# Performance work log

Measured on AMD Instinct MI355X. Metric: run time of the kernel, lower is better.

Reference implementation:

```python
import jax, jax.numpy as jnp
import numpy as np

B, N, H = 16, 8192, 128
TOK_MLP, CH_MLP = 256, 512
EPS = 1e-5


def _layer_norm(z, g, b):
    m = jnp.mean(z, axis=-1, keepdims=True)
    v = jnp.mean(jnp.square(z - m), axis=-1, keepdims=True)
    return (z - m) * jax.lax.rsqrt(v + EPS) * g + b


def setup_inputs() -> dict:
    key = jax.random.key(0)
    ks = jax.random.split(key, 9)
    s = 0.02
    return {
        "x": jax.random.normal(ks[0], (B, N, H), dtype=jnp.float32),
        "ln1_g": jnp.ones((H,), jnp.float32),
        "ln1_b": jnp.zeros((H,), jnp.float32),
        "ln2_g": jnp.ones((H,), jnp.float32),
        "ln2_b": jnp.zeros((H,), jnp.float32),
        "tok_w1": jax.random.normal(ks[1], (N, TOK_MLP), jnp.float32) * s,
        "tok_b1": jnp.zeros((TOK_MLP,), jnp.float32),
        "tok_w2": jax.random.normal(ks[2], (TOK_MLP, N), jnp.float32) * s,
        "tok_b2": jnp.zeros((N,), jnp.float32),
        "ch_w1": jax.random.normal(ks[3], (H, CH_MLP), jnp.float32) * s,
        "ch_b1": jnp.zeros((CH_MLP,), jnp.float32),
        "ch_w2": jax.random.normal(ks[4], (CH_MLP, H), jnp.float32) * s,
        "ch_b2": jnp.zeros((H,), jnp.float32),
    }


def reference(x, ln1_g, ln1_b, ln2_g, ln2_b,
              tok_w1, tok_b1, tok_w2, tok_b2,
              ch_w1, ch_b1, ch_w2, ch_b2):
    # x: [B, N, H]
    y = _layer_norm(x, ln1_g, ln1_b)
    # mask-expand-multiply-sum over dim=2 == reverse (suffix) cumsum over tokens:
    # out[b, j, h] = sum_{i >= j} y[b, i, h]
    y = jnp.flip(jnp.cumsum(jnp.flip(y, axis=1), axis=1), axis=1)  # [B, N, H]
    y = jnp.swapaxes(y, 1, 2)                                      # [B, H, N]
    h = jax.nn.gelu(y @ tok_w1 + tok_b1, approximate=False)        # [B, H, TOK_MLP]
    y = h @ tok_w2 + tok_b2                                        # [B, H, N]
    y = jnp.swapaxes(y, 1, 2)                                      # [B, N, H]
    y = _layer_norm(y, ln2_g, ln2_b)
    h = jax.nn.gelu(y @ ch_w1 + ch_b1, approximate=False)          # [B, N, CH_MLP]
    return h @ ch_w2 + ch_b2                                       # [B, N, H]
```

## Files before the change

### kernel.cpp

```cpp
#include <hip/hip_runtime.h>
#include <math.h>

#define B_ 16
#define N_ 8192
#define H_ 128
#define T_ 256
#define C_ 512

typedef __bf16 bf16x8 __attribute__((ext_vector_type(8)));
typedef __bf16 bf16x4 __attribute__((ext_vector_type(4)));
typedef float f32x4 __attribute__((ext_vector_type(4)));

__device__ __forceinline__ float gelu_f(float x) {
    float p = fmaf(0.044715f * x * x, x, x);
    float e = __expf(-1.5957691216057308f * p);
    return x * __builtin_amdgcn_rcpf(1.f + e);
}

__device__ __forceinline__ unsigned short f2bf(float x) {
    unsigned int u = __float_as_uint(x);
    u = (u + 0x7FFFu + ((u >> 16) & 1u)) >> 16;
    return (unsigned short)u;
}

__device__ __forceinline__ void gl2lds16(const void* g, void* l) {
    __builtin_amdgcn_global_load_lds(
        (const __attribute__((address_space(1))) void*)g,
        (__attribute__((address_space(3))) void*)l,
        16, 0, 0);
}

__global__ void k_w1_psum(const float* __restrict__ w1, float* __restrict__ psum) {
    int c = blockIdx.x, t = threadIdx.x;
    const float* p = w1 + (size_t)c * 64 * T_ + t;
    float s = 0.f;
    #pragma unroll 8
    for (int r = 0; r < 64; ++r) s += p[(size_t)r * T_];
    psum[c * T_ + t] = s;
}

__global__ void k_w1_scan(const float* __restrict__ psum, float* __restrict__ offs) {
    int t = threadIdx.x;
    float run = 0.f;
    for (int c = 0; c < 128; ++c) {
        offs[c * T_ + t] = run;
        run += psum[c * T_ + t];
    }
}

__global__ void k_w1_prefix(const float* __restrict__ w1, const float* __restrict__ offs,
                            unsigned short* __restrict__ w1ct) {
    int c = blockIdx.x, t = threadIdx.x;
    float run = offs[c * T_ + t];
    const float* p = w1 + (size_t)c * 64 * T_ + t;
    unsigned int wb[32];
    #pragma unroll
    for (int q = 0; q < 32; ++q) {
        run += p[(size_t)(2 * q) * T_];
        unsigned int lo = f2bf(run);
        run += p[(size_t)(2 * q + 1) * T_];
        wb[q] = lo | ((unsigned int)f2bf(run) << 16);
    }
    char* row = (char*)w1ct + ((size_t)t * N_ + c * 64) * 2;
    int key = (t & 7) << 4;
    #pragma unroll
    for (int pc = 0; pc < 8; ++pc) {
        int4 v = { (int)wb[4*pc], (int)wb[4*pc+1], (int)wb[4*pc+2], (int)wb[4*pc+3] };
        *(int4*)(row + ((pc * 16) ^ key)) = v;
    }
}

__global__ void k_packs(const float* __restrict__ w2, unsigned short* __restrict__ w2t,
                        const float* __restrict__ cw1, const float* __restrict__ cw2,
                        unsigned short* __restrict__ w1p, unsigned short* __restrict__ w2p) {
    __shared__ float ld[64 * 68];
    int tid = threadIdx.x;
    if (blockIdx.y < 4) {
        int nt = blockIdx.x, tt = blockIdx.y;
        int n0 = nt * 64, t0 = tt * 64;
        #pragma unroll
        for (int rnd = 0; rnd < 4; ++rnd) {
            int idx = tid + rnd * 256;
            int tr = idx >> 4, nc = idx & 15;
            float4 v = *(const float4*)(w2 + (size_t)(t0 + tr) * N_ + n0 + nc * 4);
            *(float4*)&ld[tr * 68 + nc * 4] = v;
        }
        __syncthreads();
        int n = tid >> 2, q = tid & 3;
        int key = (n & 7) << 4;
        unsigned int wb[8];
        #pragma unroll
        for (int j = 0; j < 8; ++j) {
            float a = ld[(q * 16 + 2 * j) * 68 + n];
            float b = ld[(q * 16 + 2 * j + 1) * 68 + n];
            wb[j] = (unsigned int)f2bf(a) | ((unsigned int)f2bf(b) << 16);
        }
        char* row = (char*)w2t + (size_t)(n0 + n) * 512 + t0 * 2;
        int4 v0 = { (int)wb[0], (int)wb[1], (int)wb[2], (int)wb[3] };
        int4 v1 = { (int)wb[4], (int)wb[5], (int)wb[6], (int)wb[7] };
        *(int4*)(row + ((q * 32) ^ key)) = v0;
        *(int4*)(row + ((q * 32 + 16) ^ key)) = v1;
    } else {
        int e = ((blockIdx.y - 4) * 128 + blockIdx.x) * 256 + tid;
        if (e < 65536) {
            int c = e >> 13, t = e & 8191;
            int n = t >> 7, j = t & 127;
            int k = j ^ ((n & 7) << 3);
            int hid = c * 64 + n;
            w1p[e] = f2bf(cw1[(size_t)k * C_ + hid]);
        } else {
            int e2 = e - 65536;
            int c = e2 >> 13, t = e2 & 8191;
            int n = t >> 6, j = t & 63;
            int k = j ^ ((n & 7) << 3);
            w2p[e2] = f2bf(cw2[(size_t)(c * 64 + k) * H_ + n]);
        }
    }
}

#define T1_YS 0
#define T1_WS 16384
#define T1_LN 81920

__global__ __launch_bounds__(1024, 1)
void k_tok1(const float* __restrict__ x, const float* __restrict__ lg,
            const float* __restrict__ lb, const unsigned short* __restrict__ w1ct,
            float* __restrict__ P) {
    __shared__ __align__(16) char sm[115712];
    float* lnb = (float*)(sm + T1_LN);
    int kk = blockIdx.x, b = blockIdx.y;
    int tid = threadIdx.x;
    int w = tid >> 6, lane = tid & 63;
    int lr = lane & 15, lk = lane >> 4;
    int mg = w >> 2, ng = w & 3;
    const char* wbg = (const char*)w1ct;
    int kbase = kk * 512;

    int rI = tid >> 4, lI = tid & 15;
    int hII = tid >> 3, segII = tid & 7;
    const float* xbase = x + ((size_t)b * N_ + kbase) * H_;

    float4 g0 = *(const float4*)(lg + lI * 8);
    float4 g1 = *(const float4*)(lg + lI * 8 + 4);
    float4 c0 = *(const float4*)(lb + lI * 8);
    float4 c1 = *(const float4*)(lb + lI * 8 + 4);

    f32x4 acc[2][4];
    #pragma unroll
    for (int i = 0; i < 2; ++i)
        #pragma unroll
        for (int j = 0; j < 4; ++j) acc[i][j] = (f32x4){0.f, 0.f, 0.f, 0.f};

    float4 xa, xb;
    auto XLOAD = [&](int t) {
        const float* p = xbase + (size_t)(t * 64 + rI) * H_ + lI * 8;
        xa = *(const float4*)p;
        xb = *(const float4*)(p + 4);
    };
    auto LNW = [&]() {
        float s1 = xa.x + xa.y + xa.z + xa.w + xb.x + xb.y + xb.z + xb.w;
        float s2 = xa.x*xa.x + xa.y*xa.y + xa.z*xa.z + xa.w*xa.w
                 + xb.x*xb.x + xb.y*xb.y + xb.z*xb.z + xb.w*xb.w;
        #pragma unroll
        for (int off = 1; off < 16; off <<= 1) {
            s1 += __shfl_xor(s1, off);
            s2 += __shfl_xor(s2, off);
        }
        float mean = s1 * (1.f / 128.f);
        float rstd = rsqrtf(s2 * (1.f / 128.f) - mean * mean + 1e-5f);
        float4 o0, o1;
        o0.x = (xa.x - mean) * rstd * g0.x + c0.x;
        o0.y = (xa.y - mean) * rstd * g0.y + c0.y;
        o0.z = (xa.z - mean) * rstd * g0.z + c0.z;
        o0.w = (xa.w - mean) * rstd * g0.w + c0.w;
        o1.x = (xb.x - mean) * rstd * g1.x + c1.x;
        o1.y = (xb.y - mean) * rstd * g1.y + c1.y;
        o1.z = (xb.z - mean) * rstd * g1.z + c1.z;
        o1.w = (xb.w - mean) * rstd * g1.w + c1.w;
        *(float4*)&lnb[rI * 132 + lI * 8]     = o0;
        *(float4*)&lnb[rI * 132 + lI * 8 + 4] = o1;
    };
    auto COLW = [&]() {
        unsigned int d[4];
        #pragma unroll
        for (int j = 0; j < 4; ++j) {
            float a = lnb[(segII * 8 + 2 * j) * 132 + hII];
            float c = lnb[(segII * 8 + 2 * j + 1) * 132 + hII];
            d[j] = (unsigned int)f2bf(a) | ((unsigned int)f2bf(c) << 16);
        }
        int4 v = { (int)d[0], (int)d[1], (int)d[2], (int)d[3] };
        *(int4*)(sm + T1_YS + hII * 128 + ((segII * 16) ^ ((hII & 7) << 4))) = v;
    };
    auto STAGEW = [&](int s, char* buf) {
        int n0 = kbase + s * 64;
        #pragma unroll
        for (int rnd = 0; rnd < 2; ++rnd) {
            int idx = tid + rnd * 1024;
            int tr = idx >> 3, pp = idx & 7;
            gl2lds16(wbg + ((size_t)tr * N_ + n0) * 2 + pp * 16, buf + idx * 16);
        }
    };

    STAGEW(0, sm + T1_WS);
    XLOAD(0);

    for (int s = 0; s < 8; ++s) {
        LNW();
        if (s < 7) XLOAD(s + 1);
        __syncthreads();
        COLW();
        __syncthreads();
        if (s < 7) STAGEW(s + 1, sm + T1_WS + ((s + 1) & 1) * 32768);
        const char* wsb = sm + T1_WS + (s & 1) * 32768;
        #pragma unroll
        for (int ks = 0; ks < 2; ++ks) {
            bf16x8 af[2], bfr[4];
            #pragma unroll
            for (int i = 0; i < 2; ++i) {
                int h = mg * 32 + i * 16 + lr;
                af[i] = *(const bf16x8*)(sm + T1_YS + h * 128 + ((ks * 64 + lk * 16) ^ ((h & 7) << 4)));
            }
            #pragma unroll
            for (int j = 0; j < 4; ++j) {
                int t = ng * 64 + j * 16 + lr;
                bfr[j] = *(const bf16x8*)(wsb + t * 128 + ((ks * 64 + lk * 16) ^ ((t & 7) << 4)));
            }
            #pragma unroll
            for (int i = 0; i < 2; ++i)
                #pragma unroll
                for (int j = 0; j < 4; ++j)
                    acc[i][j] = __builtin_amdgcn_mfma_f32_16x16x32_bf16(af[i], bfr[j], acc[i][j], 0, 0, 0);
        }
        __syncthreads();
    }

    float* Pb = P + ((size_t)(b * 16 + kk)) * (H_ * T_);
    #pragma unroll
    for (int i = 0; i < 2; ++i)
        #pragma unroll
        for (int j = 0; j < 4; ++j) {
            int t = ng * 64 + j * 16 + lr;
            #pragma unroll
            for (int r = 0; r < 4; ++r) {
                int h = mg * 32 + i * 16 + lk * 4 + r;
                Pb[h * T_ + t] = acc[i][j][r];
            }
        }
}

__global__ void k_tok1_fin(const float* __restrict__ P, const float* __restrict__ b1,
                           unsigned short* __restrict__ g1b) {
    int fid = blockIdx.x * 256 + threadIdx.x;
    int base = fid * 4;
    int b = base >> 15, rem = base & 32767;
    int h = rem >> 8, t = rem & 255;
    const float* Pb = P + (size_t)b * 16 * 32768 + rem;
    float4 a = *(const float4*)Pb;
    #pragma unroll
    for (int kk = 1; kk < 16; ++kk) {
        float4 p = *(const float4*)(Pb + (size_t)kk * 32768);
        a.x += p.x; a.y += p.y; a.z += p.z; a.w += p.w;
    }
    float4 bb = *(const float4*)(b1 + t);
    unsigned int lo = (unsigned int)f2bf(gelu_f(a.x + bb.x)) | ((unsigned int)f2bf(gelu_f(a.y + bb.y)) << 16);
    unsigned int hi = (unsigned int)f2bf(gelu_f(a.z + bb.z)) | ((unsigned int)f2bf(gelu_f(a.w + bb.w)) << 16);
    char* row = (char*)g1b + (size_t)(b * H_ + h) * 512;
    uint2 v = { lo, hi };
    *(uint2*)(row + ((t * 2) ^ ((h & 7) << 4))) = v;
}

#define F_YS 0
#define F_HS 0
#define F_W2 32768
#define F_W1 49152

__global__ __launch_bounds__(512, 4)
void k_tok2mlp(const unsigned short* __restrict__ g1b, const unsigned short* __restrict__ w2t,
               const float* __restrict__ tb2, const float* __restrict__ lg,
               const float* __restrict__ lb, const unsigned short* __restrict__ w1p,
               const unsigned short* __restrict__ w2p, const float* __restrict__ b1g,
               const float* __restrict__ b2g, float* __restrict__ out) {
    __shared__ __align__(16) char sm[65536];
    int nt = blockIdx.x, b = blockIdx.y;
    int tid = threadIdx.x;
    int w = tid >> 6, lane = tid & 63;
    int lr = lane & 15, lk = lane >> 4;
    const char* ab = (const char*)w2t + (size_t)(nt * 128) * 512;
    const char* gb = (const char*)g1b + (size_t)b * H_ * 512;
    const char* w1b = (const char*)w1p;
    const char* w2b = (const char*)w2p;

    f32x4 acc[8];
    #pragma unroll
    for (int g = 0; g < 8; ++g) acc[g] = (f32x4){0.f, 0.f, 0.f, 0.f};

    int arow = w * 16 + lr;
    int akey = (arow & 7) << 4;

    #pragma unroll
    for (int rnd = 0; rnd < 2; ++rnd) {
        int idx = tid + rnd * 512;
        int row = idx >> 3, p = idx & 7;
        gl2lds16(ab + (size_t)row * 512 + p * 16, sm + row * 128 + p * 16);
        gl2lds16(gb + (size_t)row * 512 + p * 16, sm + 16384 + row * 128 + p * 16);
    }
    __syncthreads();

    for (int q = 0; q < 4; ++q) {
        const char* cur = sm + (q & 1) * 32768;
        if (q < 3) {
            char* nxt = sm + ((q + 1) & 1) * 32768;
            #pragma unroll
            for (int rnd = 0; rnd < 2; ++rnd) {
                int idx = tid + rnd * 512;
                int row = idx >> 3, p = idx & 7;
                gl2lds16(ab + (size_t)row * 512 + (q + 1) * 128 + p * 16, nxt + row * 128 + p * 16);
                gl2lds16(gb + (size_t)row * 512 + (q + 1) * 128 + p * 16, nxt + 16384 + row * 128 + p * 16);
            }
        }
        __builtin_amdgcn_s_setprio(1);
        #pragma unroll
        for (int ks = 0; ks < 2; ++ks) {
            bf16x8 af = *(const bf16x8*)(cur + arow * 128 + ((ks * 64 + lk * 16) ^ akey));
            #pragma unroll
            for (int g = 0; g < 8; ++g) {
                int hrow = g * 16 + lr;
                bf16x8 bf_ = *(const bf16x8*)(cur + 16384 + hrow * 128 + ((ks * 64 + lk * 16) ^ ((hrow & 7) << 4)));
                acc[g] = __builtin_amdgcn_mfma_f32_16x16x32_bf16(af, bf_, acc[g], 0, 0, 0);
            }
        }
        __builtin_amdgcn_s_setprio(0);
        __syncthreads();
    }

    float gam[8], bet[8];
    #pragma unroll
    for (int g = 0; g < 8; ++g) { gam[g] = lg[g * 16 + lr]; bet[g] = lb[g * 16 + lr]; }

    #pragma unroll
    for (int j = 0; j < 2; ++j) {
        gl2lds16(w1b + w * 2048 + j * 1024 + lane * 16, sm + F_W1 + w * 2048 + j * 1024);
        gl2lds16(w2b + w * 2048 + j * 1024 + lane * 16, sm + F_W2 + w * 2048 + j * 1024);
    }

    #pragma unroll
    for (int r = 0; r < 4; ++r) {
        int row = w * 16 + lk * 4 + r;
        float bias2 = tb2[nt * 128 + row];
        float vals[8];
        float s = 0.f, ss = 0.f;
        #pragma unroll
        for (int g = 0; g < 8; ++g) {
            float v = acc[g][r] + bias2;
            vals[g] = v; s += v; ss += v * v;
        }
        #pragma unroll
        for (int off = 8; off; off >>= 1) { s += __shfl_xor(s, off); ss += __shfl_xor(ss, off); }
        float mean = s * (1.f / 128.f);
        float rstd = rsqrtf(ss * (1.f / 128.f) - mean * mean + 1e-5f);
        int key = (row & 7) << 4;
        char* orow = sm + F_YS + row * 256;
        #pragma unroll
        for (int g = 0; g < 8; ++g) {
            float v = (vals[g] - mean) * rstd * gam[g] + bet[g];
            *(unsigned short*)(orow + (((g * 16 + lr) * 2) ^ key)) = f2bf(v);
        }
    }
    __syncthreads();

    int mg = w >> 1, ng = w & 1;
    int key = (lr & 7) << 4;

    bf16x8 yfrag[2][4];
    #pragma unroll
    for (int m = 0; m < 2; ++m) {
        int yrow = (2 * mg + m) * 16 + lr;
        #pragma unroll
        for (int kc = 0; kc < 4; ++kc)
            yfrag[m][kc] = *(const bf16x8*)(sm + F_YS + yrow * 256 + ((kc * 64 + lk * 16) ^ key));
    }
    __syncthreads();

    f32x4 oacc[2][4];
    #pragma unroll
    for (int m = 0; m < 2; ++m)
        #pragma unroll
        for (int n = 0; n < 4; ++n) oacc[m][n] = (f32x4){0.f, 0.f, 0.f, 0.f};

    for (int c = 0; c < 8; ++c) {
        f32x4 hacc[2][2];
        #pragma unroll
        for (int n = 0; n < 2; ++n) {
            float4 bv4 = *(const float4*)(b1g + c * 64 + (2 * ng + n) * 16 + lk * 4);
            f32x4 iv = { bv4.x, bv4.y, bv4.z, bv4.w };
            hacc[0][n] = iv;
            hacc[1][n] = iv;
        }
        __builtin_amdgcn_s_setprio(1);
        #pragma unroll
        for (int kc = 0; kc < 4; ++kc) {
            int ko = kc * 64 + lk * 16;
            bf16x8 b0 = *(const bf16x8*)(sm + F_W1 + ((2 * ng) * 16 + lr) * 256 + (ko ^ key));
            bf16x8 b1 = *(const bf16x8*)(sm + F_W1 + ((2 * ng + 1) * 16 + lr) * 256 + (ko ^ key));
            hacc[0][0] = __builtin_amdgcn_mfma_f32_16x16x32_bf16(b0, yfrag[0][kc], hacc[0][0], 0, 0, 0);
            hacc[0][1] = __builtin_amdgcn_mfma_f32_16x16x32_bf16(b1, yfrag[0][kc], hacc[0][1], 0, 0, 0);
            hacc[1][0] = __builtin_amdgcn_mfma_f32_16x16x32_bf16(b0, yfrag[1][kc], hacc[1][0], 0, 0, 0);
            hacc[1][1] = __builtin_amdgcn_mfma_f32_16x16x32_bf16(b1, yfrag[1][kc], hacc[1][1], 0, 0, 0);
        }
        __builtin_amdgcn_s_setprio(0);
        #pragma unroll
        for (int m = 0; m < 2; ++m)
            #pragma unroll
            for (int n = 0; n < 2; ++n) {
                int tok = (2 * mg + m) * 16 + lr;
                int hid0 = (2 * ng + n) * 16 + lk * 4;
                bf16x4 pv;
                pv[0] = (__bf16)gelu_f(hacc[m][n][0]);
                pv[1] = (__bf16)gelu_f(hacc[m][n][1]);
                pv[2] = (__bf16)gelu_f(hacc[m][n][2]);
                pv[3] = (__bf16)gelu_f(hacc[m][n][3]);
                *(bf16x4*)(sm + F_HS + tok * 128 + ((hid0 * 2) ^ ((tok & 7) << 4))) = pv;
            }
        __syncthreads();
        if (c < 7) {
            #pragma unroll
            for (int j = 0; j < 2; ++j)
                gl2lds16(w1b + (c + 1) * 16384 + w * 2048 + j * 1024 + lane * 16,
                         sm + F_W1 + w * 2048 + j * 1024);
        }
        __builtin_amdgcn_s_setprio(1);
        #pragma unroll
        for (int kc = 0; kc < 2; ++kc) {
            int ko = kc * 64 + lk * 16;
            int t0 = (2 * mg) * 16 + lr, t1 = (2 * mg + 1) * 16 + lr;
            bf16x8 a0 = *(const bf16x8*)(sm + F_HS + t0 * 128 + (ko ^ ((t0 & 7) << 4)));
            bf16x8 a1 = *(const bf16x8*)(sm + F_HS + t1 * 128 + (ko ^ ((t1 & 7) << 4)));
            #pragma unroll
            for (int n = 0; n < 4; ++n) {
                bf16x8 bb = *(const bf16x8*)(sm + F_W2 + ((ng * 4 + n) * 16 + lr) * 128 + (ko ^ key));
                oacc[0][n] = __builtin_amdgcn_mfma_f32_16x16x32_bf16(a0, bb, oacc[0][n], 0, 0, 0);
                oacc[1][n] = __builtin_amdgcn_mfma_f32_16x16x32_bf16(a1, bb, oacc[1][n], 0, 0, 0);
            }
        }
        __builtin_amdgcn_s_setprio(0);
        __syncthreads();
        if (c < 7) {
            #pragma unroll
            for (int j = 0; j < 2; ++j)
                gl2lds16(w2b + (c + 1) * 16384 + w * 2048 + j * 1024 + lane * 16,
                         sm + F_W2 + w * 2048 + j * 1024);
        }
    }

    size_t rbase = (size_t)(b * 64 + nt) * 128;
    #pragma unroll
    for (int n = 0; n < 4; ++n) {
        int ch = (ng * 4 + n) * 16 + lr;
        float bv = b2g[ch];
        #pragma unroll
        for (int m = 0; m < 2; ++m)
            #pragma unroll
            for (int r = 0; r < 4; ++r) {
                size_t row = rbase + (2 * mg + m) * 16 + lk * 4 + r;
                out[row * H_ + ch] = oacc[m][n][r] + bv;
            }
    }
}

extern "C" void kernel_launch(void* const* d_in, const int* in_sizes, int n_in,
                              void* d_out, int out_size, void* d_ws, size_t ws_size,
                              hipStream_t stream) {
    const float* x      = (const float*)d_in[0];
    const float* ln1_g  = (const float*)d_in[1];
    const float* ln1_b  = (const float*)d_in[2];
    const float* ln2_g  = (const float*)d_in[3];
    const float* ln2_b  = (const float*)d_in[4];
    const float* tok_w1 = (const float*)d_in[5];
    const float* tok_b1 = (const float*)d_in[6];
    const float* tok_w2 = (const float*)d_in[7];
    const float* tok_b2 = (const float*)d_in[8];
    const float* ch_w1  = (const float*)d_in[9];
    const float* ch_b1  = (const float*)d_in[10];
    const float* ch_w2  = (const float*)d_in[11];
    const float* ch_b2  = (const float*)d_in[12];
    float* out = (float*)d_out;
    float* ws  = (float*)d_ws;

    float* psum = ws;
    float* offs = ws + 32768;
    unsigned short* w1ct = (unsigned short*)(ws + 65536);
    unsigned short* w2t  = (unsigned short*)(ws + 1114112);
    unsigned short* w1p  = (unsigned short*)(ws + 2162688);
    unsigned short* w2p  = (unsigned short*)(ws + 2195456);
    unsigned short* g1b  = (unsigned short*)(ws + 2228224);
    float* P             = ws + 2490368;

    k_w1_psum<<<dim3(128), dim3(256), 0, stream>>>(tok_w1, psum);
    k_w1_scan<<<dim3(1), dim3(256), 0, stream>>>(psum, offs);
    k_w1_prefix<<<dim3(128), dim3(256), 0, stream>>>(tok_w1, offs, w1ct);
    k_packs<<<dim3(128, 8), dim3(256), 0, stream>>>(tok_w2, w2t, ch_w1, ch_w2, w1p, w2p);
    k_tok1<<<dim3(16, 16), dim3(1024), 0, stream>>>(x, ln1_g, ln1_b, w1ct, P);
    k_tok1_fin<<<dim3(512), dim3(256), 0, stream>>>(P, tok_b1, g1b);
    k_tok2mlp<<<dim3(64, 16), dim3(512), 0, stream>>>(g1b, w2t, tok_b2, ln2_g, ln2_b,
                                                      w1p, w2p, ch_b1, ch_b2, out);
}
```

Measured before the change: 124.2 us.

## Use 32x32x16 MFMA in token-mixing GEMM and fold psum into pack kernel

The second token-MLP GEMM in k_tok2mlp now uses 32x32x16 bf16 MFMA tiles, with each wave covering 32 tokens by 64 channels, replacing the 16x16x32 tiles. Fewer fragment loads are needed per MFMA. Because each wave now holds only half of a token row, LayerNorm2 statistics are exchanged between the two waves through a small LDS table with an extra barrier. Separately, the w1 column partial-sum kernel is merged into k_packs as an extra grid row, saving one kernel launch.

```diff
diff --git a/kernel.cpp b/kernel.cpp
--- a/kernel.cpp
+++ b/kernel.cpp
@@ -10,6 +10,7 @@
 typedef __bf16 bf16x8 __attribute__((ext_vector_type(8)));
 typedef __bf16 bf16x4 __attribute__((ext_vector_type(4)));
 typedef float f32x4 __attribute__((ext_vector_type(4)));
+typedef float f32x16 __attribute__((ext_vector_type(16)));
 
 __device__ __forceinline__ float gelu_f(float x) {
     float p = fmaf(0.044715f * x * x, x, x);
@@ -28,15 +29,6 @@
         (const __attribute__((address_space(1))) void*)g,
         (__attribute__((address_space(3))) void*)l,
         16, 0, 0);
-}
-
-__global__ void k_w1_psum(const float* __restrict__ w1, float* __restrict__ psum) {
-    int c = blockIdx.x, t = threadIdx.x;
-    const float* p = w1 + (size_t)c * 64 * T_ + t;
-    float s = 0.f;
-    #pragma unroll 8
-    for (int r = 0; r < 64; ++r) s += p[(size_t)r * T_];
-    psum[c * T_ + t] = s;
 }
 
 __global__ void k_w1_scan(const float* __restrict__ psum, float* __restrict__ offs) {
@@ -72,7 +64,8 @@
 
 __global__ void k_packs(const float* __restrict__ w2, unsigned short* __restrict__ w2t,
                         const float* __restrict__ cw1, const float* __restrict__ cw2,
-                        unsigned short* __restrict__ w1p, unsigned short* __restrict__ w2p) {
+                        unsigned short* __restrict__ w1p, unsigned short* __restrict__ w2p,
+                        const float* __restrict__ w1tok, float* __restrict__ psum) {
     __shared__ float ld[64 * 68];
     int tid = threadIdx.x;
     if (blockIdx.y < 4) {
@@ -100,7 +93,7 @@
         int4 v1 = { (int)wb[4], (int)wb[5], (int)wb[6], (int)wb[7] };
         *(int4*)(row + ((q * 32) ^ key)) = v0;
         *(int4*)(row + ((q * 32 + 16) ^ key)) = v1;
-    } else {
+    } else if (blockIdx.y < 8) {
         int e = ((blockIdx.y - 4) * 128 + blockIdx.x) * 256 + tid;
         if (e < 65536) {
             int c = e >> 13, t = e & 8191;
@@ -115,6 +108,13 @@
             int k = j ^ ((n & 7) << 3);
             w2p[e2] = f2bf(cw2[(size_t)(c * 64 + k) * H_ + n]);
         }
+    } else {
+        int c = blockIdx.x, t = tid;
+        const float* p = w1tok + (size_t)c * 64 * T_ + t;
+        float s = 0.f;
+        #pragma unroll 8
+        for (int r = 0; r < 64; ++r) s += p[(size_t)r * T_];
+        psum[c * T_ + t] = s;
     }
 }
 
@@ -273,6 +273,7 @@
 #define F_HS 0
 #define F_W2 32768
 #define F_W1 49152
+#define F_TBL 32768
 
 __global__ __launch_bounds__(512, 4)
 void k_tok2mlp(const unsigned short* __restrict__ g1b, const unsigned short* __restrict__ w2t,
@@ -290,12 +291,19 @@
     const char* w1b = (const char*)w1p;
     const char* w2b = (const char*)w2p;
 
-    f32x4 acc[8];
-    #pragma unroll
-    for (int g = 0; g < 8; ++g) acc[g] = (f32x4){0.f, 0.f, 0.f, 0.f};
-
-    int arow = w * 16 + lr;
-    int akey = (arow & 7) << 4;
+    int tw = w >> 1, hw = w & 1;
+    f32x16 acc2[2];
+    #pragma unroll
+    for (int t2 = 0; t2 < 2; ++t2)
+        #pragma unroll
+        for (int i = 0; i < 16; ++i) acc2[t2][i] = 0.f;
+
+    int trow = tw * 32 + (lane & 31);
+    int hr0  = hw * 64 + (lane & 31);
+    int hr1  = hr0 + 32;
+    int tkey = (trow & 7) << 4;
+    int hkey = (hr0 & 7) << 4;
+    int kb2  = (lane >> 5) * 16;
 
     #pragma unroll
     for (int rnd = 0; rnd < 2; ++rnd) {
@@ -320,53 +328,58 @@
         }
         __builtin_amdgcn_s_setprio(1);
         #pragma unroll
-        for (int ks = 0; ks < 2; ++ks) {
-            bf16x8 af = *(const bf16x8*)(cur + arow * 128 + ((ks * 64 + lk * 16) ^ akey));
-            #pragma unroll
-            for (int g = 0; g < 8; ++g) {
-                int hrow = g * 16 + lr;
-                bf16x8 bf_ = *(const bf16x8*)(cur + 16384 + hrow * 128 + ((ks * 64 + lk * 16) ^ ((hrow & 7) << 4)));
-                acc[g] = __builtin_amdgcn_mfma_f32_16x16x32_bf16(af, bf_, acc[g], 0, 0, 0);
-            }
+        for (int s = 0; s < 4; ++s) {
+            int koff = s * 32 + kb2;
+            bf16x8 afr = *(const bf16x8*)(cur + trow * 128 + (koff ^ tkey));
+            bf16x8 b0  = *(const bf16x8*)(cur + 16384 + hr0 * 128 + (koff ^ hkey));
+            bf16x8 b1  = *(const bf16x8*)(cur + 16384 + hr1 * 128 + (koff ^ hkey));
+            acc2[0] = __builtin_amdgcn_mfma_f32_32x32x16_bf16(afr, b0, acc2[0], 0, 0, 0);
+            acc2[1] = __builtin_amdgcn_mfma_f32_32x32x16_bf16(afr, b1, acc2[1], 0, 0, 0);
         }
         __builtin_amdgcn_s_setprio(0);
         __syncthreads();
     }
 
-    float gam[8], bet[8];
-    #pragma unroll
-    for (int g = 0; g < 8; ++g) { gam[g] = lg[g * 16 + lr]; bet[g] = lb[g * 16 + lr]; }
+    float gm0 = lg[hw * 64 + (lane & 31)], gm1 = lg[hw * 64 + 32 + (lane & 31)];
+    float bt0 = lb[hw * 64 + (lane & 31)], bt1 = lb[hw * 64 + 32 + (lane & 31)];
+    float sv[16], qv[16];
+    #pragma unroll
+    for (int r = 0; r < 16; ++r) {
+        int tok = tw * 32 + (r & 3) + 8 * (r >> 2) + 4 * (lane >> 5);
+        float b2v = tb2[nt * 128 + tok];
+        float v0 = acc2[0][r] + b2v;
+        float v1 = acc2[1][r] + b2v;
+        float s = v0 + v1, qq = v0 * v0 + v1 * v1;
+        #pragma unroll
+        for (int off = 1; off < 32; off <<= 1) { s += __shfl_xor(s, off); qq += __shfl_xor(qq, off); }
+        sv[r] = s; qv[r] = qq;
+        if ((lane & 31) == 0)
+            *(float2*)(sm + F_TBL + tok * 16 + hw * 8) = (float2){ s, qq };
+    }
+    __syncthreads();
+    #pragma unroll
+    for (int r = 0; r < 16; ++r) {
+        int tok = tw * 32 + (r & 3) + 8 * (r >> 2) + 4 * (lane >> 5);
+        float2 p = *(const float2*)(sm + F_TBL + tok * 16 + (1 - hw) * 8);
+        float mean = (sv[r] + p.x) * (1.f / 128.f);
+        float var  = (qv[r] + p.y) * (1.f / 128.f) - mean * mean;
+        float rstd = rsqrtf(var + 1e-5f);
+        float b2v = tb2[nt * 128 + tok];
+        int key2 = (tok & 7) << 4;
+        char* orow = sm + F_YS + tok * 256;
+        int h0 = hw * 64 + (lane & 31);
+        float vv0 = (acc2[0][r] + b2v - mean) * rstd * gm0 + bt0;
+        float vv1 = (acc2[1][r] + b2v - mean) * rstd * gm1 + bt1;
+        *(unsigned short*)(orow + ((h0 * 2) ^ key2))        = f2bf(vv0);
+        *(unsigned short*)(orow + (((h0 + 32) * 2) ^ key2)) = f2bf(vv1);
+    }
+    __syncthreads();
 
     #pragma unroll
     for (int j = 0; j < 2; ++j) {
         gl2lds16(w1b + w * 2048 + j * 1024 + lane * 16, sm + F_W1 + w * 2048 + j * 1024);
         gl2lds16(w2b + w * 2048 + j * 1024 + lane * 16, sm + F_W2 + w * 2048 + j * 1024);
     }
-
-    #pragma unroll
-    for (int r = 0; r < 4; ++r) {
-        int row = w * 16 + lk * 4 + r;
-        float bias2 = tb2[nt * 128 + row];
-        float vals[8];
-        float s = 0.f, ss = 0.f;
-        #pragma unroll
-        for (int g = 0; g < 8; ++g) {
-            float v = acc[g][r] + bias2;
-            vals[g] = v; s += v; ss += v * v;
-        }
-        #pragma unroll
-        for (int off = 8; off; off >>= 1) { s += __shfl_xor(s, off); ss += __shfl_xor(ss, off); }
-        float mean = s * (1.f / 128.f);
-        float rstd = rsqrtf(ss * (1.f / 128.f) - mean * mean + 1e-5f);
-        int key = (row & 7) << 4;
-        char* orow = sm + F_YS + row * 256;
-        #pragma unroll
-        for (int g = 0; g < 8; ++g) {
-            float v = (vals[g] - mean) * rstd * gam[g] + bet[g];
-            *(unsigned short*)(orow + (((g * 16 + lr) * 2) ^ key)) = f2bf(v);
-        }
-    }
-    __syncthreads();
 
     int mg = w >> 1, ng = w & 1;
     int key = (lr & 7) << 4;
@@ -495,10 +508,10 @@
     unsigned short* g1b  = (unsigned short*)(ws + 2228224);
     float* P             = ws + 2490368;
 
-    k_w1_psum<<<dim3(128), dim3(256), 0, stream>>>(tok_w1, psum);
+    k_packs<<<dim3(128, 9), dim3(256), 0, stream>>>(tok_w2, w2t, ch_w1, ch_w2, w1p, w2p,
+                                                    tok_w1, psum);
     k_w1_scan<<<dim3(1), dim3(256), 0, stream>>>(psum, offs);
     k_w1_prefix<<<dim3(128), dim3(256), 0, stream>>>(tok_w1, offs, w1ct);
-    k_packs<<<dim3(128, 8), dim3(256), 0, stream>>>(tok_w2, w2t, ch_w1, ch_w2, w1p, w2p);
     k_tok1<<<dim3(16, 16), dim3(1024), 0, stream>>>(x, ln1_g, ln1_b, w1ct, P);
     k_tok1_fin<<<dim3(512), dim3(256), 0, stream>>>(P, tok_b1, g1b);
     k_tok2mlp<<<dim3(64, 16), dim3(512), 0, stream>>>(g1b, w2t, tok_b2, ln2_g, ln2_b,
```

Result: slower. 132.3 us (+6.5%).
